# Optimization experiments

Hardware: AMD Instinct MI355X
Metric: run time of the kernel (lower is better)

## Reference

```python
import jax, jax.numpy as jnp
import numpy as np

BATCH, SEQ, DIM = 256, 80, 1024
HEADS = 8
HID = 4 * DIM
EPS = 1e-5


def _ln(x, g, b):
    mu = jnp.mean(x, axis=-1, keepdims=True)
    var = jnp.mean((x - mu) ** 2, axis=-1, keepdims=True)
    return (x - mu) * jax.lax.rsqrt(var + EPS) * g + b


def setup_inputs() -> dict:
    key = jax.random.key(0)
    ks = jax.random.split(key, 8)
    w = lambda k, shape: jax.random.normal(k, shape, dtype=jnp.float32) * 0.02
    return {
        "x": jax.random.normal(ks[0], (BATCH, SEQ, DIM), dtype=jnp.float32),
        "Wq": w(ks[1], (DIM, DIM)),
        "Wk": w(ks[2], (DIM, DIM)),
        "Wv": w(ks[3], (DIM, DIM)),
        "bias_table": w(ks[4], (2 * SEQ - 1, HEADS)),
        "to_out_g": jnp.ones((DIM,), jnp.float32),
        "to_out_b": jnp.zeros((DIM,), jnp.float32),
        "ln1_g": jnp.ones((DIM,), jnp.float32),
        "ln1_b": jnp.zeros((DIM,), jnp.float32),
        "ln2_g": jnp.ones((DIM,), jnp.float32),
        "ln2_b": jnp.zeros((DIM,), jnp.float32),
        "fc1_w": w(ks[5], (DIM, HID)),
        "fc1_b": jnp.zeros((HID,), jnp.float32),
        "fc2_w": w(ks[6], (HID, DIM)),
        "fc2_b": jnp.zeros((DIM,), jnp.float32),
    }


def reference(x, Wq, Wk, Wv, bias_table, to_out_g, to_out_b,
              ln1_g, ln1_b, ln2_g, ln2_b, fc1_w, fc1_b, fc2_w, fc2_b):
    B, S, E = x.shape
    H = HEADS
    D = E // H
    scale = E ** (-0.5)  # NOTE: full emb_size scale, faithful to source

    q = (x @ Wq).reshape(B, S, H, D).transpose(0, 2, 1, 3)  # bhsd
    k = (x @ Wk).reshape(B, S, H, D).transpose(0, 2, 1, 3)
    v = (x @ Wv).reshape(B, S, H, D).transpose(0, 2, 1, 3)

    attn = jnp.einsum('bhqd,bhkd->bhqk', q, k) * scale
    attn = jax.nn.softmax(attn, axis=-1)

    # relative bias added AFTER softmax (non-standard, faithful)
    idx = jnp.arange(S)[:, None] - jnp.arange(S)[None, :] + (S - 1)  # [S,S] in [0,2S-2]
    bias = bias_table[idx].transpose(2, 0, 1)  # (H, S, S)
    attn = attn + bias[None]

    out = jnp.einsum('bhqk,bhkd->bhqd', attn, v)
    out = out.transpose(0, 2, 1, 3).reshape(B, S, E)
    out = _ln(out, to_out_g, to_out_b)  # LayerNorm inside attention (to_out)

    x = _ln(x + out, ln1_g, ln1_b)      # post-norm residual 1
    h = jax.nn.gelu(x @ fc1_w + fc1_b, approximate=False)  # torch nn.GELU exact
    ff = h @ fc2_w + fc2_b
    return _ln(x + ff, ln2_g, ln2_b)    # post-norm residual 2
```

## Files before the change

kernel.cpp:

```cpp
#include <hip/hip_runtime.h>
#include <stdint.h>

#define BATCH 256
#define SEQ   80
#define DIM   1024
#define HEADS 8
#define HDIM  128
#define HID   4096
#define NTOK  (BATCH * SEQ)

typedef unsigned short u16;
using short8_t = __attribute__((ext_vector_type(8))) short;
using f32x4    = __attribute__((ext_vector_type(4))) float;

__device__ __forceinline__ u16 f2bf(float f) {
  unsigned u = __float_as_uint(f);
  u += 0x7fffu + ((u >> 16) & 1u);
  return (u16)(u >> 16);
}
__device__ __forceinline__ float bf2f(u16 u) {
  return __uint_as_float(((unsigned)u) << 16);
}

__device__ __forceinline__ float gelu_exact(float v) {
  return 0.5f * v * (1.0f + erff(v * 0.70710678118654752f));
}

#define GLD16(gp, lp)                                                   \
  __builtin_amdgcn_global_load_lds(                                     \
      (__attribute__((address_space(1))) void*)(void*)(gp),             \
      (__attribute__((address_space(3))) void*)(void*)(lp), 16, 0, 0)

__global__ __launch_bounds__(256) void cast_bf16_kernel(
    const float* __restrict__ in, u16* __restrict__ out, int n4) {
  int i = blockIdx.x * 256 + threadIdx.x;
  int stride = gridDim.x * 256;
  for (; i < n4; i += stride) {
    float4 v = ((const float4*)in)[i];
    uint2 o;
    o.x = (unsigned)f2bf(v.x) | ((unsigned)f2bf(v.y) << 16);
    o.y = (unsigned)f2bf(v.z) | ((unsigned)f2bf(v.w) << 16);
    ((uint2*)out)[i] = o;
  }
}

__global__ __launch_bounds__(256) void transpose_cast_kernel(
    const float* __restrict__ in, u16* __restrict__ out, int R, int C) {
  __shared__ float tile[32][33];
  int c0 = blockIdx.x * 32, r0 = blockIdx.y * 32;
  for (int k = 0; k < 4; k++) {
    int i = threadIdx.y + k * 8;
    tile[i][threadIdx.x] = in[(size_t)(r0 + i) * C + c0 + threadIdx.x];
  }
  __syncthreads();
  for (int k = 0; k < 4; k++) {
    int i = threadIdx.y + k * 8;
    out[(size_t)(c0 + i) * R + r0 + threadIdx.x] = f2bf(tile[threadIdx.x][i]);
  }
}

template <int EPI>
__global__ __launch_bounds__(512, 2) void gemm8p(
    const u16* __restrict__ A, const u16* __restrict__ Bt,
    const float* __restrict__ bias, u16* __restrict__ outp,
    int M, int N, int K, int ntn) {
  __shared__ __align__(16) u16 lds[65536];

  const int tid = threadIdx.x;
  const int lane = tid & 63, wave = tid >> 6;
  const int wm = wave >> 2, wn = wave & 3;
  const int lo = lane & 15, hi = lane >> 4;

  const int nwg = gridDim.x;
  int q8 = nwg >> 3, r8 = nwg & 7;
  int xcd = blockIdx.x & 7, off = blockIdx.x >> 3;
  int swz = (xcd < r8 ? xcd * (q8 + 1) : r8 * (q8 + 1) + (xcd - r8) * q8) + off;
  const int bn = swz % ntn, bm = swz / ntn;
  const size_t arow0 = (size_t)bm * 256, bcol0 = (size_t)bn * 256;

  const int srow = tid >> 2;
  const int slb  = (tid & 3) ^ ((srow >> 1) & 3);
  const u16* sA = A + (arow0 + srow) * K + slb * 8;
  const u16* sB = Bt + (bcol0 + srow) * K + slb * 8;
  const size_t sstep = 128 * (size_t)K;

  const int arow = wm * 128 + lo;
  const int brow = wn * 64 + lo;
  const int aoff = arow * 32 + (hi ^ ((arow >> 1) & 3)) * 8;
  const int boff = brow * 32 + (hi ^ ((brow >> 1) & 3)) * 8;

  f32x4 acc[8][4] = {};
  const int NT = K >> 6;
  const int NI = NT >> 1;

#define STG(mat, buf, kh, t)                                                  \
  do {                                                                        \
    const u16* s_ = ((mat) ? sB : sA) + (size_t)(t) * 64 + (kh) * 32;         \
    u16* d_ = lds + ((((buf) << 2) | ((mat) << 1) | (kh)) << 13) + wave * 512;\
    GLD16(s_, d_);                                                            \
    GLD16(s_ + sstep, d_ + 4096);                                             \
  } while (0)

#define RD_A(buf, kh, mh, dst)                                                \
  _Pragma("unroll") for (int mi = 0; mi < 4; ++mi)                            \
      dst[mi] = *(const short8_t*)&lds[((((buf) << 2) | (kh)) << 13) + aoff + \
                                       ((mh) * 4 + mi) * 512];

#define RD_B(buf, kh, dst)                                                    \
  _Pragma("unroll") for (int ni = 0; ni < 4; ++ni)                            \
      dst[ni] = *(const short8_t*)&lds[((((buf) << 2) | 2 | (kh)) << 13) +    \
                                       boff + ni * 512];

#define MFMA16(mh, a_, b_)                                                    \
  __builtin_amdgcn_s_setprio(1);                                              \
  _Pragma("unroll") for (int mi = 0; mi < 4; ++mi)                            \
  _Pragma("unroll") for (int ni = 0; ni < 4; ++ni)                            \
      acc[(mh) * 4 + mi][ni] = __builtin_amdgcn_mfma_f32_16x16x32_bf16(       \
          a_[mi], b_[ni], acc[(mh) * 4 + mi][ni], 0, 0, 0);                   \
  __builtin_amdgcn_s_setprio(0);

#define BAR()   asm volatile("s_barrier" ::: "memory")
#define LGKM0() asm volatile("s_waitcnt lgkmcnt(0)" ::: "memory")
#define VM10()  asm volatile("s_waitcnt vmcnt(10)" ::: "memory")

  STG(1, 0, 0, 0); STG(0, 0, 0, 0); STG(1, 0, 1, 0); STG(0, 0, 1, 0);
  STG(1, 1, 0, 1); STG(0, 1, 0, 1); STG(1, 1, 1, 1);
  asm volatile("s_waitcnt vmcnt(0)" ::: "memory");
  BAR();

  for (int i = 0; i < NI; ++i) {
    const int t0 = 2 * i, t1 = 2 * i + 1;
    const bool s0 = (t0 + 2 < NT), s1 = (t1 + 2 < NT);
    short8_t a[4], b[4];
    RD_A(0, 0, 0, a); RD_B(0, 0, b);
    STG(0, 1, 1, t1);
    BAR(); LGKM0(); MFMA16(0, a, b); BAR();
    RD_A(0, 0, 1, a);
    if (s0) STG(1, 0, 0, t0 + 2);
    BAR(); LGKM0(); MFMA16(1, a, b); VM10(); BAR();
    RD_A(0, 1, 0, a); RD_B(0, 1, b);
    if (s0) STG(0, 0, 0, t0 + 2);
    BAR(); LGKM0(); MFMA16(0, a, b); BAR();
    RD_A(0, 1, 1, a);
    if (s0) STG(1, 0, 1, t0 + 2);
    BAR(); LGKM0(); MFMA16(1, a, b); VM10(); BAR();
    RD_A(1, 0, 0, a); RD_B(1, 0, b);
    if (s0) STG(0, 0, 1, t0 + 2);
    BAR(); LGKM0(); MFMA16(0, a, b); BAR();
    RD_A(1, 0, 1, a);
    if (s1) STG(1, 1, 0, t1 + 2);
    BAR(); LGKM0(); MFMA16(1, a, b); VM10(); BAR();
    RD_A(1, 1, 0, a); RD_B(1, 1, b);
    if (s1) STG(0, 1, 0, t1 + 2);
    BAR(); LGKM0(); MFMA16(0, a, b); BAR();
    RD_A(1, 1, 1, a);
    if (s1) STG(1, 1, 1, t1 + 2);
    BAR(); LGKM0(); MFMA16(1, a, b); VM10(); BAR();
  }
#undef STG
#undef RD_A
#undef RD_B
#undef MFMA16

  asm volatile("s_waitcnt vmcnt(0)" ::: "memory");
  __syncthreads();

  u16* ct = lds;
#pragma unroll
  for (int n = 0; n < 4; ++n) {
    int col = wn * 64 + n * 16 + lo;
    float bv = 0.f;
    if constexpr (EPI != 0) bv = bias[bcol0 + col];
#pragma unroll
    for (int m = 0; m < 8; ++m) {
#pragma unroll
      for (int j = 0; j < 4; ++j) {
        int row = wm * 128 + m * 16 + hi * 4 + j;
        float v = acc[m][n][j] + bv;
        if constexpr (EPI == 1) v = gelu_exact(v);
        ct[row * 256 + col] = f2bf(v);
      }
    }
  }
  __syncthreads();
  u16* op = outp + arow0 * (size_t)N + bcol0;
#pragma unroll
  for (int i = 0; i < 16; ++i) {
    int c = i * 512 + tid;
    int row = c >> 5, o2 = (c & 31) * 8;
    *(short8_t*)(op + (size_t)row * N + o2) = *(const short8_t*)&ct[row * 256 + o2];
  }
}

__global__ __launch_bounds__(64) void attn_kernel(
    const u16* __restrict__ QKV, const float* __restrict__ bias_table,
    u16* __restrict__ attnout) {
  __shared__ __align__(16) u16 Kt[80 * 128];
  __shared__ __align__(16) u16 Vt[96 * 128];
  __shared__ float bias_l[159];

  const int bh = blockIdx.x;
  const int b = bh >> 3, h = bh & 7;
  const int lane = threadIdx.x, lo = lane & 15, hi = lane >> 4;
  const size_t tokbase = (size_t)b * SEQ * 3072;
  const u16* Qg = QKV + tokbase + h * HDIM;
  const u16* Kg = QKV + tokbase + 1024 + h * HDIM;
  const u16* Vg = QKV + tokbase + 2048 + h * HDIM;

#pragma unroll
  for (int i = 0; i < 20; i++) {
    int flat = i * 64 + lane;
    int row = flat >> 4;
    int col = (flat & 15) * 8;
    GLD16(Kg + (size_t)row * 3072 + col, &Kt[i * 512]);
    GLD16(Vg + (size_t)row * 3072 + col, &Vt[i * 512]);
  }
  for (int i = lane; i < 16 * 128; i += 64) Vt[80 * 128 + i] = 0;
  for (int i = lane; i < 159; i += 64) bias_l[i] = bias_table[i * 8 + h];
  asm volatile("s_waitcnt vmcnt(0)" ::: "memory");
  __syncthreads();

  f32x4 sa[5][5] = {};
#pragma unroll
  for (int ks = 0; ks < 4; ks++) {
    short8_t ak[5], bq[5];
#pragma unroll
    for (int m = 0; m < 5; m++)
      ak[m] = *(const short8_t*)&Kt[(m * 16 + lo) * 128 + ks * 32 + hi * 8];
#pragma unroll
    for (int n = 0; n < 5; n++)
      bq[n] = *(const short8_t*)(Qg + (size_t)(n * 16 + lo) * 3072 + ks * 32 + hi * 8);
#pragma unroll
    for (int m = 0; m < 5; m++)
#pragma unroll
      for (int n = 0; n < 5; n++)
        sa[m][n] = __builtin_amdgcn_mfma_f32_16x16x32_bf16(ak[m], bq[n], sa[m][n], 0, 0, 0);
  }
  __syncthreads();

  u16* p_lds = Kt;
  for (int i = lane; i < 80 * 16; i += 64) {
    int q = i >> 4, c = 80 + (i & 15);
    p_lds[q * 104 + c] = 0;
  }
  const float scale = 0.03125f;
#pragma unroll
  for (int n = 0; n < 5; n++) {
    float mx = -1e30f;
#pragma unroll
    for (int m = 0; m < 5; m++)
#pragma unroll
      for (int j = 0; j < 4; j++) {
        sa[m][n][j] *= scale;
        mx = fmaxf(mx, sa[m][n][j]);
      }
    mx = fmaxf(mx, __shfl_xor(mx, 16));
    mx = fmaxf(mx, __shfl_xor(mx, 32));
    float sm = 0.f;
#pragma unroll
    for (int m = 0; m < 5; m++)
#pragma unroll
      for (int j = 0; j < 4; j++) {
        float e = __expf(sa[m][n][j] - mx);
        sa[m][n][j] = e;
        sm += e;
      }
    sm += __shfl_xor(sm, 16);
    sm += __shfl_xor(sm, 32);
    float inv = 1.0f / sm;
    int q = n * 16 + lo;
#pragma unroll
    for (int m = 0; m < 5; m++)
#pragma unroll
      for (int j = 0; j < 4; j++) {
        int key = m * 16 + hi * 4 + j;
        float pv = sa[m][n][j] * inv + bias_l[q - key + 79];
        p_lds[q * 104 + key] = f2bf(pv);
      }
  }
  __syncthreads();

#pragma unroll
  for (int half = 0; half < 2; half++) {
    f32x4 oa[5][4] = {};
#pragma unroll
    for (int ks = 0; ks < 3; ks++) {
      short8_t ap[5];
#pragma unroll
      for (int m = 0; m < 5; m++)
        ap[m] = *(const short8_t*)&p_lds[(m * 16 + lo) * 104 + ks * 32 + hi * 8];
      short8_t bv[4];
#pragma unroll
      for (int nd = 0; nd < 4; nd++) {
        int d = (half * 4 + nd) * 16 + lo;
        short8_t tt;
#pragma unroll
        for (int j = 0; j < 8; j++)
          tt[j] = (short)Vt[(ks * 32 + hi * 8 + j) * 128 + d];
        bv[nd] = tt;
      }
#pragma unroll
      for (int m = 0; m < 5; m++)
#pragma unroll
        for (int nd = 0; nd < 4; nd++)
          oa[m][nd] = __builtin_amdgcn_mfma_f32_16x16x32_bf16(ap[m], bv[nd], oa[m][nd], 0, 0, 0);
    }
#pragma unroll
    for (int m = 0; m < 5; m++)
#pragma unroll
      for (int nd = 0; nd < 4; nd++)
#pragma unroll
        for (int j = 0; j < 4; j++) {
          int q = m * 16 + hi * 4 + j;
          int d = (half * 4 + nd) * 16 + lo;
          attnout[((size_t)b * SEQ + q) * DIM + h * HDIM + d] = f2bf(oa[m][nd][j]);
        }
  }
}

__device__ __forceinline__ void block_reduce2(float& a, float& b, float* sbuf) {
#pragma unroll
  for (int m = 1; m < 64; m <<= 1) {
    a += __shfl_xor(a, m);
    b += __shfl_xor(b, m);
  }
  int w = threadIdx.x >> 6;
  if ((threadIdx.x & 63) == 0) { sbuf[w * 2] = a; sbuf[w * 2 + 1] = b; }
  __syncthreads();
  a = sbuf[0] + sbuf[2] + sbuf[4] + sbuf[6];
  b = sbuf[1] + sbuf[3] + sbuf[5] + sbuf[7];
  __syncthreads();
}

__global__ __launch_bounds__(256) void fuse1_kernel(
    const u16* __restrict__ attnout, const float* __restrict__ x,
    const float* __restrict__ og, const float* __restrict__ ob,
    const float* __restrict__ g1, const float* __restrict__ b1,
    u16* __restrict__ x1b) {
  __shared__ float sbuf[8];
  const size_t base = (size_t)blockIdx.x * DIM;
  float a[4], r[4];
  float s0 = 0.f, s1 = 0.f;
#pragma unroll
  for (int i = 0; i < 4; i++) {
    int idx = threadIdx.x + i * 256;
    a[i] = bf2f(attnout[base + idx]);
    s0 += a[i];
    s1 += a[i] * a[i];
  }
  block_reduce2(s0, s1, sbuf);
  float mu = s0 * (1.f / DIM);
  float rstd = rsqrtf(s1 * (1.f / DIM) - mu * mu + 1e-5f);
  float t0 = 0.f, t1 = 0.f;
#pragma unroll
  for (int i = 0; i < 4; i++) {
    int idx = threadIdx.x + i * 256;
    float o = (a[i] - mu) * rstd * og[idx] + ob[idx];
    r[i] = x[base + idx] + o;
    t0 += r[i];
    t1 += r[i] * r[i];
  }
  block_reduce2(t0, t1, sbuf);
  float mu2 = t0 * (1.f / DIM);
  float rstd2 = rsqrtf(t1 * (1.f / DIM) - mu2 * mu2 + 1e-5f);
#pragma unroll
  for (int i = 0; i < 4; i++) {
    int idx = threadIdx.x + i * 256;
    x1b[base + idx] = f2bf((r[i] - mu2) * rstd2 * g1[idx] + b1[idx]);
  }
}

__global__ __launch_bounds__(256) void fuse2_kernel(
    const u16* __restrict__ x1b, const u16* __restrict__ ff,
    const float* __restrict__ g2, const float* __restrict__ b2,
    float* __restrict__ out) {
  __shared__ float sbuf[8];
  const size_t base = (size_t)blockIdx.x * DIM;
  float r[4];
  float s0 = 0.f, s1 = 0.f;
#pragma unroll
  for (int i = 0; i < 4; i++) {
    int idx = threadIdx.x + i * 256;
    r[i] = bf2f(x1b[base + idx]) + bf2f(ff[base + idx]);
    s0 += r[i];
    s1 += r[i] * r[i];
  }
  block_reduce2(s0, s1, sbuf);
  float mu = s0 * (1.f / DIM);
  float rstd = rsqrtf(s1 * (1.f / DIM) - mu * mu + 1e-5f);
#pragma unroll
  for (int i = 0; i < 4; i++) {
    int idx = threadIdx.x + i * 256;
    out[base + idx] = (r[i] - mu) * rstd * g2[idx] + b2[idx];
  }
}

extern "C" void kernel_launch(void* const* d_in, const int* in_sizes, int n_in,
                              void* d_out, int out_size, void* d_ws, size_t ws_size,
                              hipStream_t stream) {
  const float* x        = (const float*)d_in[0];
  const float* Wq       = (const float*)d_in[1];
  const float* Wk       = (const float*)d_in[2];
  const float* Wv       = (const float*)d_in[3];
  const float* bias_tab = (const float*)d_in[4];
  const float* og       = (const float*)d_in[5];
  const float* ob       = (const float*)d_in[6];
  const float* g1       = (const float*)d_in[7];
  const float* b1       = (const float*)d_in[8];
  const float* g2       = (const float*)d_in[9];
  const float* b2       = (const float*)d_in[10];
  const float* fc1w     = (const float*)d_in[11];
  const float* fc1b     = (const float*)d_in[12];
  const float* fc2w     = (const float*)d_in[13];
  const float* fc2b     = (const float*)d_in[14];

  char* ws = (char*)d_ws;
  u16* wqkvT = (u16*)(ws + 0);
  u16* fc1T  = (u16*)(ws + 6291456ull);
  u16* fc2T  = (u16*)(ws + 14680064ull);
  u16* pbuf  = (u16*)(ws + 23068672ull);
  u16* qbuf  = (u16*)(ws + 65011712ull);
  char* cbuf = ws + 106954752ull;
  size_t cavail = ws_size > 106954752ull ? ws_size - 106954752ull : 0;

  int cb = 1;
  while (cb < 16 && (size_t)(BATCH / cb) * SEQ * 3072 * 2 > cavail) cb <<= 1;
  int cf = 1;
  while (cf < 16 && (size_t)(NTOK / cf) * HID * 2 > cavail) cf <<= 1;

  dim3 tb(32, 8);
  cast_bf16_kernel<<<2048, 256, 0, stream>>>(x, qbuf, NTOK * DIM / 4);
  transpose_cast_kernel<<<dim3(32, 32), tb, 0, stream>>>(Wq, wqkvT, 1024, 1024);
  transpose_cast_kernel<<<dim3(32, 32), tb, 0, stream>>>(Wk, wqkvT + 1024 * 1024, 1024, 1024);
  transpose_cast_kernel<<<dim3(32, 32), tb, 0, stream>>>(Wv, wqkvT + 2 * 1024 * 1024, 1024, 1024);
  transpose_cast_kernel<<<dim3(128, 32), tb, 0, stream>>>(fc1w, fc1T, 1024, 4096);
  transpose_cast_kernel<<<dim3(32, 128), tb, 0, stream>>>(fc2w, fc2T, 4096, 1024);

  {
    const int nb = BATCH / cb;
    const int rows = nb * SEQ;
    u16* qkvc = (u16*)cbuf;
    const int nwg = (rows / 256) * (3072 / 256);
    for (int c = 0; c < cb; ++c) {
      const u16* xb_c = qbuf + (size_t)c * rows * DIM;
      gemm8p<0><<<nwg, 512, 0, stream>>>(xb_c, wqkvT, nullptr, qkvc,
                                         rows, 3072, 1024, 3072 / 256);
      attn_kernel<<<nb * HEADS, 64, 0, stream>>>(
          qkvc, bias_tab, pbuf + (size_t)c * rows * DIM);
    }
  }

  fuse1_kernel<<<NTOK, 256, 0, stream>>>(pbuf, x, og, ob, g1, b1, qbuf);

  {
    const int rows = NTOK / cf;
    u16* hc = (u16*)cbuf;
    const int nwg1 = (rows / 256) * (HID / 256);
    const int nwg2 = (rows / 256) * (DIM / 256);
    for (int c = 0; c < cf; ++c) {
      gemm8p<1><<<nwg1, 512, 0, stream>>>(qbuf + (size_t)c * rows * DIM, fc1T,
                                          fc1b, hc, rows, HID, 1024, HID / 256);
      gemm8p<2><<<nwg2, 512, 0, stream>>>(hc, fc2T, fc2b,
                                          pbuf + (size_t)c * rows * DIM,
                                          rows, 1024, HID, DIM / 256);
    }
  }

  fuse2_kernel<<<NTOK, 256, 0, stream>>>(qbuf, pbuf, g2, b2, (float*)d_out);
}
```

Measured before the change: 808.9 us.

## Restructure GEMM main loop with double-buffered register fragments and fewer barriers

Rewrites the GEMM inner loop so LDS fragment reads for the next MFMA block go into alternate register sets while the current block computes. About half of the per-phase barriers are removed, and the vmcnt waits are retuned. The final iteration is peeled into its own epilogue, which drops the per-stage bounds checks from the steady-state loop. This raises register pressure and depends on subtle ordering of LDS buffer reuse for correctness.

```diff
diff --git a/kernel.cpp b/kernel.cpp
--- a/kernel.cpp
+++ b/kernel.cpp
@@ -121,41 +121,78 @@
 
 #define BAR()   asm volatile("s_barrier" ::: "memory")
 #define LGKM0() asm volatile("s_waitcnt lgkmcnt(0)" ::: "memory")
-#define VM10()  asm volatile("s_waitcnt vmcnt(10)" ::: "memory")
-
-  STG(1, 0, 0, 0); STG(0, 0, 0, 0); STG(1, 0, 1, 0); STG(0, 0, 1, 0);
-  STG(1, 1, 0, 1); STG(0, 1, 0, 1); STG(1, 1, 1, 1);
+#define VM(n)   asm volatile("s_waitcnt vmcnt(" #n ")" ::: "memory")
+
+  STG(0, 0, 0, 0); STG(1, 0, 0, 0); STG(0, 0, 1, 0); STG(1, 0, 1, 0);
+  STG(0, 1, 0, 1); STG(1, 1, 0, 1); STG(1, 1, 1, 1);
   asm volatile("s_waitcnt vmcnt(0)" ::: "memory");
   BAR();
 
-  for (int i = 0; i < NI; ++i) {
+  short8_t aR0[4], aR1[4], bR0[4], bR1[4];
+
+  for (int i = 0; i < NI - 1; ++i) {
     const int t0 = 2 * i, t1 = 2 * i + 1;
-    const bool s0 = (t0 + 2 < NT), s1 = (t1 + 2 < NT);
-    short8_t a[4], b[4];
-    RD_A(0, 0, 0, a); RD_B(0, 0, b);
+    RD_A(0, 0, 0, aR0); RD_B(0, 0, bR0);
+    LGKM0(); MFMA16(0, aR0, bR0);
+    RD_A(0, 0, 1, aR1);
     STG(0, 1, 1, t1);
-    BAR(); LGKM0(); MFMA16(0, a, b); BAR();
-    RD_A(0, 0, 1, a);
-    if (s0) STG(1, 0, 0, t0 + 2);
-    BAR(); LGKM0(); MFMA16(1, a, b); VM10(); BAR();
-    RD_A(0, 1, 0, a); RD_B(0, 1, b);
-    if (s0) STG(0, 0, 0, t0 + 2);
-    BAR(); LGKM0(); MFMA16(0, a, b); BAR();
-    RD_A(0, 1, 1, a);
-    if (s0) STG(1, 0, 1, t0 + 2);
-    BAR(); LGKM0(); MFMA16(1, a, b); VM10(); BAR();
-    RD_A(1, 0, 0, a); RD_B(1, 0, b);
-    if (s0) STG(0, 0, 1, t0 + 2);
-    BAR(); LGKM0(); MFMA16(0, a, b); BAR();
-    RD_A(1, 0, 1, a);
-    if (s1) STG(1, 1, 0, t1 + 2);
-    BAR(); LGKM0(); MFMA16(1, a, b); VM10(); BAR();
-    RD_A(1, 1, 0, a); RD_B(1, 1, b);
-    if (s1) STG(0, 1, 0, t1 + 2);
-    BAR(); LGKM0(); MFMA16(0, a, b); BAR();
-    RD_A(1, 1, 1, a);
-    if (s1) STG(1, 1, 1, t1 + 2);
-    BAR(); LGKM0(); MFMA16(1, a, b); VM10(); BAR();
+    VM(8); BAR();
+    LGKM0(); MFMA16(1, aR1, bR0);
+    RD_A(0, 1, 0, aR0); RD_B(0, 1, bR1);
+    STG(1, 0, 0, t0 + 2);
+    BAR();
+    LGKM0(); MFMA16(0, aR0, bR1);
+    RD_A(0, 1, 1, aR1);
+    STG(0, 0, 0, t0 + 2);
+    VM(8); BAR();
+    LGKM0(); MFMA16(1, aR1, bR1);
+    RD_A(1, 0, 0, aR0); RD_B(1, 0, bR0);
+    STG(1, 0, 1, t0 + 2);
+    BAR();
+    LGKM0(); MFMA16(0, aR0, bR0);
+    RD_A(1, 0, 1, aR1);
+    STG(0, 0, 1, t0 + 2);
+    VM(8); BAR();
+    LGKM0(); MFMA16(1, aR1, bR0);
+    RD_A(1, 1, 0, aR0); RD_B(1, 1, bR1);
+    STG(1, 1, 0, t1 + 2);
+    BAR();
+    LGKM0(); MFMA16(0, aR0, bR1);
+    RD_A(1, 1, 1, aR1);
+    STG(0, 1, 0, t1 + 2);
+    BAR();
+    LGKM0(); MFMA16(1, aR1, bR1);
+    STG(1, 1, 1, t1 + 2);
+    VM(10); BAR();
+  }
+
+  {
+    const int t1 = NT - 1;
+    RD_A(0, 0, 0, aR0); RD_B(0, 0, bR0);
+    LGKM0(); MFMA16(0, aR0, bR0);
+    RD_A(0, 0, 1, aR1);
+    STG(0, 1, 1, t1);
+    VM(8); BAR();
+    LGKM0(); MFMA16(1, aR1, bR0);
+    RD_A(0, 1, 0, aR0); RD_B(0, 1, bR1);
+    BAR();
+    LGKM0(); MFMA16(0, aR0, bR1);
+    RD_A(0, 1, 1, aR1);
+    VM(4); BAR();
+    LGKM0(); MFMA16(1, aR1, bR1);
+    RD_A(1, 0, 0, aR0); RD_B(1, 0, bR0);
+    BAR();
+    LGKM0(); MFMA16(0, aR0, bR0);
+    RD_A(1, 0, 1, aR1);
+    VM(0); BAR();
+    LGKM0(); MFMA16(1, aR1, bR0);
+    RD_A(1, 1, 0, aR0); RD_B(1, 1, bR1);
+    BAR();
+    LGKM0(); MFMA16(0, aR0, bR1);
+    RD_A(1, 1, 1, aR1);
+    BAR();
+    LGKM0(); MFMA16(1, aR1, bR1);
+    BAR();
   }
 #undef STG
 #undef RD_A
```

Result: faster. 759.5 us (-6.1%).

## Restructure GEMM pipeline into 4 phases and split-K the fc2 GEMM

Applied to the files above, without the earlier changes.

Replaces the 8-phase half-tile MFMA schedule with 4 phases that each read the full A/B fragments and issue 32 MFMAs per barrier pair. The change halves the barrier count and loads both matrices per stage. Adds split-K by two for the fc2 GEMM: each K-half writes its own bf16 partial buffer, and fuse2 sums the partials plus the fc2 bias. fuse2 now runs per chunk. This raises fc2 workgroup count for better CU fill, in exchange for extra partial-buffer traffic and bf16 rounding of the partials. The larger register fragments risk higher VGPR pressure.

```diff
diff --git a/kernel.cpp b/kernel.cpp
--- a/kernel.cpp
+++ b/kernel.cpp
@@ -60,10 +60,10 @@
 }
 
 template <int EPI>
-__global__ __launch_bounds__(512, 2) void gemm8p(
+__global__ __launch_bounds__(512, 2) void gemm4p(
     const u16* __restrict__ A, const u16* __restrict__ Bt,
-    const float* __restrict__ bias, u16* __restrict__ outp,
-    int M, int N, int K, int ntn) {
+    const float* __restrict__ bias, u16* __restrict__ outp, u16* __restrict__ outp1,
+    int M, int N, int Keff, int Ks, int ntn, int ntm) {
   __shared__ __align__(16) u16 lds[65536];
 
   const int tid = threadIdx.x;
@@ -75,14 +75,17 @@
   int q8 = nwg >> 3, r8 = nwg & 7;
   int xcd = blockIdx.x & 7, off = blockIdx.x >> 3;
   int swz = (xcd < r8 ? xcd * (q8 + 1) : r8 * (q8 + 1) + (xcd - r8) * q8) + off;
-  const int bn = swz % ntn, bm = swz / ntn;
+  const int per = ntn * ntm;
+  const int kp = swz / per, rem = swz % per;
+  const int bn = rem % ntn, bm = rem / ntn;
   const size_t arow0 = (size_t)bm * 256, bcol0 = (size_t)bn * 256;
+  const int kbase = kp * Keff;
 
   const int srow = tid >> 2;
   const int slb  = (tid & 3) ^ ((srow >> 1) & 3);
-  const u16* sA = A + (arow0 + srow) * K + slb * 8;
-  const u16* sB = Bt + (bcol0 + srow) * K + slb * 8;
-  const size_t sstep = 128 * (size_t)K;
+  const u16* sA = A + (arow0 + srow) * (size_t)Ks + kbase + slb * 8;
+  const u16* sB = Bt + (bcol0 + srow) * (size_t)Ks + kbase + slb * 8;
+  const size_t sstep = 128 * (size_t)Ks;
 
   const int arow = wm * 128 + lo;
   const int brow = wn * 64 + lo;
@@ -90,7 +93,7 @@
   const int boff = brow * 32 + (hi ^ ((brow >> 1) & 3)) * 8;
 
   f32x4 acc[8][4] = {};
-  const int NT = K >> 6;
+  const int NT = Keff >> 6;
   const int NI = NT >> 1;
 
 #define STG(mat, buf, kh, t)                                                  \
@@ -101,66 +104,70 @@
     GLD16(s_ + sstep, d_ + 4096);                                             \
   } while (0)
 
-#define RD_A(buf, kh, mh, dst)                                                \
-  _Pragma("unroll") for (int mi = 0; mi < 4; ++mi)                            \
+#define RD_A8(buf, kh, dst)                                                   \
+  _Pragma("unroll") for (int mi = 0; mi < 8; ++mi)                            \
       dst[mi] = *(const short8_t*)&lds[((((buf) << 2) | (kh)) << 13) + aoff + \
-                                       ((mh) * 4 + mi) * 512];
-
-#define RD_B(buf, kh, dst)                                                    \
+                                       mi * 512];
+
+#define RD_B4(buf, kh, dst)                                                   \
   _Pragma("unroll") for (int ni = 0; ni < 4; ++ni)                            \
       dst[ni] = *(const short8_t*)&lds[((((buf) << 2) | 2 | (kh)) << 13) +    \
                                        boff + ni * 512];
 
-#define MFMA16(mh, a_, b_)                                                    \
+#define MFMA32(a_, b_)                                                        \
   __builtin_amdgcn_s_setprio(1);                                              \
-  _Pragma("unroll") for (int mi = 0; mi < 4; ++mi)                            \
+  _Pragma("unroll") for (int mi = 0; mi < 8; ++mi)                            \
   _Pragma("unroll") for (int ni = 0; ni < 4; ++ni)                            \
-      acc[(mh) * 4 + mi][ni] = __builtin_amdgcn_mfma_f32_16x16x32_bf16(       \
-          a_[mi], b_[ni], acc[(mh) * 4 + mi][ni], 0, 0, 0);                   \
+      acc[mi][ni] = __builtin_amdgcn_mfma_f32_16x16x32_bf16(                  \
+          a_[mi], b_[ni], acc[mi][ni], 0, 0, 0);                              \
   __builtin_amdgcn_s_setprio(0);
 
 #define BAR()   asm volatile("s_barrier" ::: "memory")
 #define LGKM0() asm volatile("s_waitcnt lgkmcnt(0)" ::: "memory")
-#define VM10()  asm volatile("s_waitcnt vmcnt(10)" ::: "memory")
-
-  STG(1, 0, 0, 0); STG(0, 0, 0, 0); STG(1, 0, 1, 0); STG(0, 0, 1, 0);
-  STG(1, 1, 0, 1); STG(0, 1, 0, 1); STG(1, 1, 1, 1);
+
+#define PHASE(buf, kh, aR, bR, STGCODE, VMASM)                                \
+  do {                                                                        \
+    RD_A8(buf, kh, aR);                                                       \
+    RD_B4(buf, kh, bR);                                                       \
+    STGCODE;                                                                  \
+    asm volatile(VMASM ::: "memory");                                         \
+    BAR();                                                                    \
+    LGKM0();                                                                  \
+    MFMA32(aR, bR);                                                           \
+  } while (0)
+
+  STG(0, 0, 0, 0); STG(1, 0, 0, 0);
+  STG(0, 0, 1, 0); STG(1, 0, 1, 0);
+  STG(0, 1, 0, 1); STG(1, 1, 0, 1);
   asm volatile("s_waitcnt vmcnt(0)" ::: "memory");
   BAR();
 
-  for (int i = 0; i < NI; ++i) {
+  short8_t aX[8], bX[4], aY[8], bY[4];
+
+  for (int i = 0; i < NI - 1; ++i) {
     const int t0 = 2 * i, t1 = 2 * i + 1;
-    const bool s0 = (t0 + 2 < NT), s1 = (t1 + 2 < NT);
-    short8_t a[4], b[4];
-    RD_A(0, 0, 0, a); RD_B(0, 0, b);
-    STG(0, 1, 1, t1);
-    BAR(); LGKM0(); MFMA16(0, a, b); BAR();
-    RD_A(0, 0, 1, a);
-    if (s0) STG(1, 0, 0, t0 + 2);
-    BAR(); LGKM0(); MFMA16(1, a, b); VM10(); BAR();
-    RD_A(0, 1, 0, a); RD_B(0, 1, b);
-    if (s0) STG(0, 0, 0, t0 + 2);
-    BAR(); LGKM0(); MFMA16(0, a, b); BAR();
-    RD_A(0, 1, 1, a);
-    if (s0) STG(1, 0, 1, t0 + 2);
-    BAR(); LGKM0(); MFMA16(1, a, b); VM10(); BAR();
-    RD_A(1, 0, 0, a); RD_B(1, 0, b);
-    if (s0) STG(0, 0, 1, t0 + 2);
-    BAR(); LGKM0(); MFMA16(0, a, b); BAR();
-    RD_A(1, 0, 1, a);
-    if (s1) STG(1, 1, 0, t1 + 2);
-    BAR(); LGKM0(); MFMA16(1, a, b); VM10(); BAR();
-    RD_A(1, 1, 0, a); RD_B(1, 1, b);
-    if (s1) STG(0, 1, 0, t1 + 2);
-    BAR(); LGKM0(); MFMA16(0, a, b); BAR();
-    RD_A(1, 1, 1, a);
-    if (s1) STG(1, 1, 1, t1 + 2);
-    BAR(); LGKM0(); MFMA16(1, a, b); VM10(); BAR();
-  }
+    PHASE(0, 0, aX, bX, { STG(0, 1, 1, t1);     STG(1, 1, 1, t1); },
+          "s_waitcnt vmcnt(8)");
+    PHASE(0, 1, aY, bY, { STG(0, 0, 0, t0 + 2); STG(1, 0, 0, t0 + 2); },
+          "s_waitcnt vmcnt(8)");
+    PHASE(1, 0, aX, bX, { STG(0, 0, 1, t0 + 2); STG(1, 0, 1, t0 + 2); },
+          "s_waitcnt vmcnt(8)");
+    PHASE(1, 1, aY, bY, { STG(0, 1, 0, t1 + 2); STG(1, 1, 0, t1 + 2); },
+          "s_waitcnt vmcnt(8)");
+  }
+  {
+    const int t1 = NT - 1;
+    PHASE(0, 0, aX, bX, { STG(0, 1, 1, t1); STG(1, 1, 1, t1); },
+          "s_waitcnt vmcnt(8)");
+    PHASE(0, 1, aY, bY, {}, "s_waitcnt vmcnt(4)");
+    PHASE(1, 0, aX, bX, {}, "s_waitcnt vmcnt(0)");
+    PHASE(1, 1, aY, bY, {}, "");
+  }
+#undef PHASE
 #undef STG
-#undef RD_A
-#undef RD_B
-#undef MFMA16
+#undef RD_A8
+#undef RD_B4
+#undef MFMA32
 
   asm volatile("s_waitcnt vmcnt(0)" ::: "memory");
   __syncthreads();
@@ -183,7 +190,7 @@
     }
   }
   __syncthreads();
-  u16* op = outp + arow0 * (size_t)N + bcol0;
+  u16* op = (kp ? outp1 : outp) + arow0 * (size_t)N + bcol0;
 #pragma unroll
   for (int i = 0; i < 16; ++i) {
     int c = i * 512 + tid;
@@ -371,7 +378,8 @@
 }
 
 __global__ __launch_bounds__(256) void fuse2_kernel(
-    const u16* __restrict__ x1b, const u16* __restrict__ ff,
+    const u16* __restrict__ x1b, const u16* __restrict__ p0,
+    const u16* __restrict__ p1, const float* __restrict__ fc2b,
     const float* __restrict__ g2, const float* __restrict__ b2,
     float* __restrict__ out) {
   __shared__ float sbuf[8];
@@ -381,7 +389,8 @@
 #pragma unroll
   for (int i = 0; i < 4; i++) {
     int idx = threadIdx.x + i * 256;
-    r[i] = bf2f(x1b[base + idx]) + bf2f(ff[base + idx]);
+    r[i] = bf2f(x1b[base + idx]) + bf2f(p0[base + idx]) + bf2f(p1[base + idx]) +
+           fc2b[idx];
     s0 += r[i];
     s1 += r[i] * r[i];
   }
@@ -426,7 +435,7 @@
   int cb = 1;
   while (cb < 16 && (size_t)(BATCH / cb) * SEQ * 3072 * 2 > cavail) cb <<= 1;
   int cf = 1;
-  while (cf < 16 && (size_t)(NTOK / cf) * HID * 2 > cavail) cf <<= 1;
+  while (cf < 16 && (size_t)(NTOK / cf) * (HID + DIM) * 2 > cavail) cf <<= 1;
 
   dim3 tb(32, 8);
   cast_bf16_kernel<<<2048, 256, 0, stream>>>(x, qbuf, NTOK * DIM / 4);
@@ -440,11 +449,12 @@
     const int nb = BATCH / cb;
     const int rows = nb * SEQ;
     u16* qkvc = (u16*)cbuf;
-    const int nwg = (rows / 256) * (3072 / 256);
+    const int ntm = rows / 256;
+    const int nwg = ntm * 12;
     for (int c = 0; c < cb; ++c) {
       const u16* xb_c = qbuf + (size_t)c * rows * DIM;
-      gemm8p<0><<<nwg, 512, 0, stream>>>(xb_c, wqkvT, nullptr, qkvc,
-                                         rows, 3072, 1024, 3072 / 256);
+      gemm4p<0><<<nwg, 512, 0, stream>>>(xb_c, wqkvT, nullptr, qkvc, qkvc,
+                                         rows, 3072, 1024, 1024, 12, ntm);
       attn_kernel<<<nb * HEADS, 64, 0, stream>>>(
           qkvc, bias_tab, pbuf + (size_t)c * rows * DIM);
     }
@@ -454,17 +464,18 @@
 
   {
     const int rows = NTOK / cf;
-    u16* hc = (u16*)cbuf;
-    const int nwg1 = (rows / 256) * (HID / 256);
-    const int nwg2 = (rows / 256) * (DIM / 256);
+    u16* hc  = (u16*)cbuf;
+    u16* p1c = (u16*)(cbuf + (size_t)rows * HID * 2);
+    const int ntm = rows / 256;
     for (int c = 0; c < cf; ++c) {
-      gemm8p<1><<<nwg1, 512, 0, stream>>>(qbuf + (size_t)c * rows * DIM, fc1T,
-                                          fc1b, hc, rows, HID, 1024, HID / 256);
-      gemm8p<2><<<nwg2, 512, 0, stream>>>(hc, fc2T, fc2b,
-                                          pbuf + (size_t)c * rows * DIM,
-                                          rows, 1024, HID, DIM / 256);
+      const size_t off = (size_t)c * rows * DIM;
+      gemm4p<1><<<ntm * 16, 512, 0, stream>>>(qbuf + off, fc1T, fc1b, hc, hc,
+                                              rows, HID, 1024, 1024, 16, ntm);
+      gemm4p<0><<<ntm * 4 * 2, 512, 0, stream>>>(hc, fc2T, nullptr,
+                                                 pbuf + off, p1c,
+                                                 rows, 1024, 2048, 4096, 4, ntm);
+      fuse2_kernel<<<rows, 256, 0, stream>>>(qbuf + off, pbuf + off, p1c, fc2b,
+                                             g2, b2, (float*)d_out + off);
     }
   }
-
-  fuse2_kernel<<<NTOK, 256, 0, stream>>>(qbuf, pbuf, g2, b2, (float*)d_out);
-}
+}
```

Result: faster. 764.3 us (-5.5%).
